# Kernel optimization log

Measured on AMD Instinct MI355X. Metric: run time of the kernel, lower is better.

The kernel has to match this reference:

```python
import jax, jax.numpy as jnp
import numpy as np

N = 8192      # collocation points
H = 128       # hidden width of the stream-function MLP


def setup_inputs() -> dict:
    key = jax.random.key(0)
    ks = jax.random.split(key, 9)
    s = lambda fan_in: 1.0 / np.sqrt(fan_in)
    return {
        "x":  jax.random.normal(ks[0], (N, 3), dtype=jnp.float32),
        "W1": jax.random.normal(ks[1], (3, H), dtype=jnp.float32) * s(3),
        "b1": jnp.zeros((H,), dtype=jnp.float32),
        "W2": jax.random.normal(ks[2], (H, H), dtype=jnp.float32) * s(H),
        "b2": jnp.zeros((H,), dtype=jnp.float32),
        "W3": jax.random.normal(ks[3], (H, H), dtype=jnp.float32) * s(H),
        "b3": jnp.zeros((H,), dtype=jnp.float32),
        "W4": jax.random.normal(ks[4], (H, 1), dtype=jnp.float32) * s(H),
        "b4": jnp.zeros((1,), dtype=jnp.float32),
        "nu": jnp.float32(1.0),
    }


def reference(x, W1, b1, W2, b2, W3, b3, W4, b4, nu):
    # psi: scalar stream function of a single sample xi = (x, y, t)
    def psi(xi):
        h = jnp.tanh(xi @ W1 + b1)
        h = jnp.tanh(h @ W2 + b2)
        h = jnp.tanh(h @ W3 + b3)
        return (h @ W4 + b4)[0]

    # vorticity w = dv/dx - du/dy = -(psi_xx + psi_yy)
    def w_fn(xi):
        Hpsi = jax.hessian(psi)(xi)          # [3,3]
        return -(Hpsi[0, 0] + Hpsi[1, 1])

    def per_sample(xi):
        g = jax.grad(psi)(xi)                # dpsi: [3]
        u = g[1]
        v = -g[0]
        dw = jax.grad(w_fn)(xi)              # [dwdx, dwdy, dwdt]
        Hw = jax.hessian(w_fn)(xi)           # 4th-order derivs of psi
        lapw = Hw[0, 0] + Hw[1, 1]
        nse = dw[2] + dw[0] * u + dw[1] * v - nu * lapw
        return jnp.stack([u, v]), nse

    f, NSE = jax.vmap(per_sample)(x)         # f: [N,2], NSE: [N]
    return f, NSE
```

## Files before the change

### kernel.cpp

```cpp
#include <hip/hip_runtime.h>
#include <hip/hip_bf16.h>

#define NSAMP 8192
#define HD 128
#define NC 18
#define SB 8
#define NCOLS 144
#define KSTR 136

typedef __attribute__((ext_vector_type(8))) short bf16x8;
typedef __attribute__((ext_vector_type(4))) float f32x4;
typedef float f2 __attribute__((ext_vector_type(2)));


__device__ __forceinline__ unsigned packf2(f2 v) {
    __hip_bfloat162 h = __float22bfloat162_rn(float2{v.x, v.y});
    return *(unsigned*)&h;
}
__device__ __forceinline__ f2 unpk(unsigned r) {
    f2 v;
    v.x = __uint_as_float(r << 16);
    v.y = __uint_as_float(r & 0xffff0000u);
    return v;
}

__device__ __forceinline__ void jmul2(const f2* __restrict__ p,
                                      const f2* __restrict__ q,
                                      f2* __restrict__ r) {
    r[0]  = p[0]*q[0];
    r[1]  = p[0]*q[1]  + p[1]*q[0];
    r[2]  = p[0]*q[2]  + p[2]*q[0];
    r[3]  = p[0]*q[3]  + p[3]*q[0];
    r[4]  = p[0]*q[4]  + p[4]*q[0]  + p[1]*q[1];
    r[5]  = p[0]*q[5]  + p[5]*q[0]  + p[1]*q[2]  + p[2]*q[1];
    r[6]  = p[0]*q[6]  + p[6]*q[0]  + p[2]*q[2];
    r[7]  = p[0]*q[7]  + p[7]*q[0]  + p[1]*q[3]  + p[3]*q[1];
    r[8]  = p[0]*q[8]  + p[8]*q[0]  + p[2]*q[3]  + p[3]*q[2];
    r[9]  = p[0]*q[9]  + p[9]*q[0]  + p[1]*q[4]  + p[4]*q[1];
    r[10] = p[0]*q[10] + p[10]*q[0] + p[1]*q[5]  + p[5]*q[1] + p[2]*q[4] + p[4]*q[2];
    r[11] = p[0]*q[11] + p[11]*q[0] + p[1]*q[6]  + p[6]*q[1] + p[2]*q[5] + p[5]*q[2];
    r[12] = p[0]*q[12] + p[12]*q[0] + p[2]*q[6]  + p[6]*q[2];
    r[13] = p[0]*q[13] + p[13]*q[0] + p[1]*q[7]  + p[7]*q[1] + p[3]*q[4] + p[4]*q[3];
    r[14] = p[0]*q[14] + p[14]*q[0] + p[2]*q[8]  + p[8]*q[2] + p[3]*q[6] + p[6]*q[3];
    r[15] = p[0]*q[15] + p[15]*q[0] + p[1]*q[9]  + p[9]*q[1] + p[4]*q[4];
    r[16] = p[0]*q[16] + p[16]*q[0] + p[1]*q[11] + p[11]*q[1] + p[2]*q[10] + p[10]*q[2]
          + p[4]*q[6]  + p[6]*q[4]  + p[5]*q[5];
    r[17] = p[0]*q[17] + p[17]*q[0] + p[2]*q[12] + p[12]*q[2] + p[6]*q[6];
}

__device__ __forceinline__ void tanh_jet2(const f2* __restrict__ f,
                                          f2* __restrict__ out) {
    f2 y;  y.x = tanhf(f[0].x);  y.y = tanhf(f[0].y);
    const f2 one = {1.0f, 1.0f};
    const f2 s  = one - y*y;
    const f2 t2 = -y*s;
    const f2 t3 = s*(y*y - 0.3333333333333333f);
    const f2 t4 = y*s*(one + one - 3.0f*y*y) * 0.3333333333333333f;
    f2 p[NC], A[NC], B[NC];
    p[0] = (f2)0.0f;
#pragma unroll
    for (int i = 1; i < NC; ++i) p[i] = f[i];
    A[0] = t3;
#pragma unroll
    for (int i = 1; i < NC; ++i) A[i] = t4 * p[i];
    jmul2(p, A, B);  B[0] += t2;
    jmul2(p, B, A);  A[0] += s;
    jmul2(p, A, out); out[0] += y;
}

__global__ __launch_bounds__(512, 4)
void hydro_main(const float* __restrict__ x,
                const float* __restrict__ W1, const float* __restrict__ b1,
                const float* __restrict__ W2, const float* __restrict__ b2,
                const float* __restrict__ W3, const float* __restrict__ b3,
                const float* __restrict__ W4, const float* __restrict__ nu_p,
                float* __restrict__ out) {
    __shared__ __align__(16) unsigned short Hl[NCOLS * KSTR];
    __shared__ float psis[NCOLS];

    const int tid = threadIdx.x;
    const int wv  = tid >> 6;
    const int ln  = tid & 63;
    const int s0  = blockIdx.x * SB;
    const int s   = tid >> 6;
    const int jp  = tid & 63;

    {
        const float xs = x[3 * (s0 + s) + 0];
        const float ys = x[3 * (s0 + s) + 1];
        const float ts = x[3 * (s0 + s) + 2];
        const int j0 = 2 * jp;
        const f2 wx = *(const f2*)&W1[j0];
        const f2 wy = *(const f2*)&W1[HD + j0];
        const f2 wt = *(const f2*)&W1[2 * HD + j0];
        const f2 bb = *(const f2*)&b1[j0];
        f2 f[NC], h[NC];
#pragma unroll
        for (int c = 0; c < NC; ++c) f[c] = (f2)0.0f;
        f[0] = wx * xs + wy * ys + wt * ts + bb;
        f[1] = wx; f[2] = wy; f[3] = wt;
        tanh_jet2(f, h);
#pragma unroll
        for (int c = 0; c < NC; ++c)
            *(unsigned*)&Hl[(s * NC + c) * KSTR + j0] = packf2(h[c]);
    }
    __syncthreads();

#pragma unroll 1
    for (int L = 0; L < 2; ++L) {
        const float* __restrict__ W = L ? W3 : W2;
        const int jj   = 16 * wv + (ln & 15);
        const int koff = (ln >> 4) * 8;
        bf16x8 Af[4];
#pragma unroll
        for (int ks = 0; ks < 4; ++ks) {
            union { uint4 u; bf16x8 v; } cv;
            const int kb = ks * 32 + koff;
            cv.u.x = packf2(f2{W[(kb + 0) * HD + jj], W[(kb + 1) * HD + jj]});
            cv.u.y = packf2(f2{W[(kb + 2) * HD + jj], W[(kb + 3) * HD + jj]});
            cv.u.z = packf2(f2{W[(kb + 4) * HD + jj], W[(kb + 5) * HD + jj]});
            cv.u.w = packf2(f2{W[(kb + 6) * HD + jj], W[(kb + 7) * HD + jj]});
            Af[ks] = cv.v;
        }
        f32x4 acc[9];
#pragma unroll
        for (int nt = 0; nt < 9; ++nt) acc[nt] = (f32x4)0.0f;
#pragma unroll
        for (int ks = 0; ks < 4; ++ks) {
#pragma unroll
            for (int nt = 0; nt < 9; ++nt) {
                const bf16x8 Bf = *(const bf16x8*)&Hl[(nt * 16 + (ln & 15)) * KSTR + ks * 32 + koff];
                acc[nt] = __builtin_amdgcn_mfma_f32_16x16x32_bf16(Af[ks], Bf, acc[nt], 0, 0, 0);
            }
        }
        __syncthreads();
#pragma unroll
        for (int nt = 0; nt < 9; ++nt) {
            const int n = nt * 16 + (ln & 15);
            const int m = 16 * wv + (ln >> 4) * 4;
            uint2 w;
            w.x = packf2(f2{acc[nt].x, acc[nt].y});
            w.y = packf2(f2{acc[nt].z, acc[nt].w});
            *(uint2*)&Hl[n * KSTR + m] = w;
        }
        __syncthreads();
        {
            const float* bL = L ? b3 : b2;
            const int j0 = 2 * jp;
            f2 fa[NC], ha[NC];
#pragma unroll
            for (int c = 0; c < NC; ++c)
                fa[c] = unpk(*(const unsigned*)&Hl[(s * NC + c) * KSTR + j0]);
            fa[0] += *(const f2*)&bL[j0];
            tanh_jet2(fa, ha);
#pragma unroll
            for (int c = 0; c < NC; ++c)
                *(unsigned*)&Hl[(s * NC + c) * KSTR + j0] = packf2(ha[c]);
        }
        __syncthreads();
    }

    if (tid < NCOLS) {
        float acc = 0.0f;
#pragma unroll
        for (int kk = 0; kk < 16; ++kk) {
            const uint4 q = *(const uint4*)&Hl[tid * KSTR + kk * 8];
            const int k = kk * 8;
            const f2 e0 = unpk(q.x), e1 = unpk(q.y), e2 = unpk(q.z), e3 = unpk(q.w);
            acc = fmaf(e0.x, W4[k + 0], acc);
            acc = fmaf(e0.y, W4[k + 1], acc);
            acc = fmaf(e1.x, W4[k + 2], acc);
            acc = fmaf(e1.y, W4[k + 3], acc);
            acc = fmaf(e2.x, W4[k + 4], acc);
            acc = fmaf(e2.y, W4[k + 5], acc);
            acc = fmaf(e3.x, W4[k + 6], acc);
            acc = fmaf(e3.y, W4[k + 7], acc);
        }
        psis[tid] = acc;
    }
    __syncthreads();

    if (tid < SB) {
        const float* p = &psis[tid * NC];
        const float nu = nu_p[0];
        const float u  = p[2];
        const float v  = -p[1];
        const float wx = -(6.0f * p[9]  + 2.0f * p[11]);
        const float wy = -(2.0f * p[10] + 6.0f * p[12]);
        const float wt = -(2.0f * p[13] + 2.0f * p[14]);
        const float lapw = -(24.0f * p[15] + 8.0f * p[16] + 24.0f * p[17]);
        const float nse  = wt + wx * u + wy * v - nu * lapw;
        const int gi = s0 + tid;
        out[2 * gi]         = u;
        out[2 * gi + 1]     = v;
        out[2 * NSAMP + gi] = nse;
    }
}

extern "C" void kernel_launch(void* const* d_in, const int* in_sizes, int n_in,
                              void* d_out, int out_size, void* d_ws, size_t ws_size,
                              hipStream_t stream) {
    const float* x  = (const float*)d_in[0];
    const float* W1 = (const float*)d_in[1];
    const float* b1 = (const float*)d_in[2];
    const float* W2 = (const float*)d_in[3];
    const float* b2 = (const float*)d_in[4];
    const float* W3 = (const float*)d_in[5];
    const float* b3 = (const float*)d_in[6];
    const float* W4 = (const float*)d_in[7];
    const float* nu = (const float*)d_in[9];
    float* out = (float*)d_out;

    hipLaunchKernelGGL(hydro_main, dim3(NSAMP / SB), dim3(512), 0, stream,
                       x, W1, b1, W2, b2, W3, b3, W4, nu, out);
}
```

Before: 100.8 us.

## Retile hidden-layer MFMA as 32x80 per wave and halve tanh-jet threads

Each wave now computes a 32-row by 5-column-tile block of the hidden-layer GEMM instead of 16 rows by 9 tiles. Each B fragment loaded from LDS therefore feeds two MFMAs, and the weight fragments are loaded per k-step inside a non-unrolled loop rather than all up front. Column tile 4 is computed by both column halves, which adds some redundant MFMA work. The tanh-jet stage now runs on only 256 threads, each handling four hidden units with wider LDS loads. This trades parallelism and latency hiding in the heaviest elementwise phase for fewer LDS transactions, and may lower register pressure.

```diff
diff --git a/kernel.cpp b/kernel.cpp
--- a/kernel.cpp
+++ b/kernel.cpp
@@ -82,10 +82,10 @@
     const int wv  = tid >> 6;
     const int ln  = tid & 63;
     const int s0  = blockIdx.x * SB;
-    const int s   = tid >> 6;
-    const int jp  = tid & 63;
 
     {
+        const int s  = tid >> 6;
+        const int jp = tid & 63;
         const float xs = x[3 * (s0 + s) + 0];
         const float ys = x[3 * (s0 + s) + 1];
         const float ts = x[3 * (s0 + s) + 2];
@@ -106,56 +106,78 @@
     }
     __syncthreads();
 
+    const int half = wv & 1;
+    const int ntb  = half * 4;
+    const int mg   = wv >> 1;
+    const int mr0  = mg * 32 + (ln & 15);
+    const int koff = (ln >> 4) * 8;
+
 #pragma unroll 1
     for (int L = 0; L < 2; ++L) {
         const float* __restrict__ W = L ? W3 : W2;
-        const int jj   = 16 * wv + (ln & 15);
-        const int koff = (ln >> 4) * 8;
-        bf16x8 Af[4];
-#pragma unroll
+        f32x4 acc[2][5];
+#pragma unroll
+        for (int mt = 0; mt < 2; ++mt)
+#pragma unroll
+            for (int t = 0; t < 5; ++t) acc[mt][t] = (f32x4)0.0f;
+
+#pragma unroll 1
         for (int ks = 0; ks < 4; ++ks) {
-            union { uint4 u; bf16x8 v; } cv;
             const int kb = ks * 32 + koff;
-            cv.u.x = packf2(f2{W[(kb + 0) * HD + jj], W[(kb + 1) * HD + jj]});
-            cv.u.y = packf2(f2{W[(kb + 2) * HD + jj], W[(kb + 3) * HD + jj]});
-            cv.u.z = packf2(f2{W[(kb + 4) * HD + jj], W[(kb + 5) * HD + jj]});
-            cv.u.w = packf2(f2{W[(kb + 6) * HD + jj], W[(kb + 7) * HD + jj]});
-            Af[ks] = cv.v;
-        }
-        f32x4 acc[9];
-#pragma unroll
-        for (int nt = 0; nt < 9; ++nt) acc[nt] = (f32x4)0.0f;
-#pragma unroll
-        for (int ks = 0; ks < 4; ++ks) {
-#pragma unroll
-            for (int nt = 0; nt < 9; ++nt) {
-                const bf16x8 Bf = *(const bf16x8*)&Hl[(nt * 16 + (ln & 15)) * KSTR + ks * 32 + koff];
-                acc[nt] = __builtin_amdgcn_mfma_f32_16x16x32_bf16(Af[ks], Bf, acc[nt], 0, 0, 0);
+            union { uint4 u; bf16x8 v; } a0, a1;
+            a0.u.x = packf2(f2{W[(kb + 0) * HD + mr0], W[(kb + 1) * HD + mr0]});
+            a0.u.y = packf2(f2{W[(kb + 2) * HD + mr0], W[(kb + 3) * HD + mr0]});
+            a0.u.z = packf2(f2{W[(kb + 4) * HD + mr0], W[(kb + 5) * HD + mr0]});
+            a0.u.w = packf2(f2{W[(kb + 6) * HD + mr0], W[(kb + 7) * HD + mr0]});
+            a1.u.x = packf2(f2{W[(kb + 0) * HD + mr0 + 16], W[(kb + 1) * HD + mr0 + 16]});
+            a1.u.y = packf2(f2{W[(kb + 2) * HD + mr0 + 16], W[(kb + 3) * HD + mr0 + 16]});
+            a1.u.z = packf2(f2{W[(kb + 4) * HD + mr0 + 16], W[(kb + 5) * HD + mr0 + 16]});
+            a1.u.w = packf2(f2{W[(kb + 6) * HD + mr0 + 16], W[(kb + 7) * HD + mr0 + 16]});
+#pragma unroll
+            for (int t = 0; t < 5; ++t) {
+                const int n = (ntb + t) * 16 + (ln & 15);
+                const bf16x8 Bf = *(const bf16x8*)&Hl[n * KSTR + kb];
+                acc[0][t] = __builtin_amdgcn_mfma_f32_16x16x32_bf16(a0.v, Bf, acc[0][t], 0, 0, 0);
+                acc[1][t] = __builtin_amdgcn_mfma_f32_16x16x32_bf16(a1.v, Bf, acc[1][t], 0, 0, 0);
             }
         }
         __syncthreads();
 #pragma unroll
-        for (int nt = 0; nt < 9; ++nt) {
-            const int n = nt * 16 + (ln & 15);
-            const int m = 16 * wv + (ln >> 4) * 4;
-            uint2 w;
-            w.x = packf2(f2{acc[nt].x, acc[nt].y});
-            w.y = packf2(f2{acc[nt].z, acc[nt].w});
-            *(uint2*)&Hl[n * KSTR + m] = w;
+        for (int t = 0; t < 5; ++t) {
+            const int n  = (ntb + t) * 16 + (ln & 15);
+            const int m0 = mg * 32 + (ln >> 4) * 4;
+            uint2 w0, w1;
+            w0.x = packf2(f2{acc[0][t].x, acc[0][t].y});
+            w0.y = packf2(f2{acc[0][t].z, acc[0][t].w});
+            w1.x = packf2(f2{acc[1][t].x, acc[1][t].y});
+            w1.y = packf2(f2{acc[1][t].z, acc[1][t].w});
+            *(uint2*)&Hl[n * KSTR + m0]      = w0;
+            *(uint2*)&Hl[n * KSTR + m0 + 16] = w1;
         }
         __syncthreads();
-        {
+        if (tid < 256) {
             const float* bL = L ? b3 : b2;
-            const int j0 = 2 * jp;
-            f2 fa[NC], ha[NC];
-#pragma unroll
-            for (int c = 0; c < NC; ++c)
-                fa[c] = unpk(*(const unsigned*)&Hl[(s * NC + c) * KSTR + j0]);
+            const int s  = tid >> 5;
+            const int q  = tid & 31;
+            const int j0 = 4 * q;
+            f2 fa[NC], fb[NC], ha[NC], hb[NC];
+#pragma unroll
+            for (int c = 0; c < NC; ++c) {
+                const uint2 u = *(const uint2*)&Hl[(s * NC + c) * KSTR + j0];
+                fa[c] = unpk(u.x);
+                fb[c] = unpk(u.y);
+            }
             fa[0] += *(const f2*)&bL[j0];
+            fb[0] += *(const f2*)&bL[j0 + 2];
             tanh_jet2(fa, ha);
-#pragma unroll
-            for (int c = 0; c < NC; ++c)
-                *(unsigned*)&Hl[(s * NC + c) * KSTR + j0] = packf2(ha[c]);
+            tanh_jet2(fb, hb);
+#pragma unroll
+            for (int c = 0; c < NC; ++c) {
+                uint2 w;
+                w.x = packf2(ha[c]);
+                w.y = packf2(hb[c]);
+                *(uint2*)&Hl[(s * NC + c) * KSTR + j0] = w;
+            }
         }
         __syncthreads();
     }
```

New measurement: 105.7 us. +4.9%, slower.
